# Optimization experiments

Hardware: AMD Instinct MI355X
Metric: run time of the kernel (lower is better)

Reference implementation:

```python
import jax, jax.numpy as jnp
import numpy as np
from jax import lax

WINDOW = 9
PAD = WINDOW // 2
LAMBDA_REG = 1.0
DN = lax.conv_dimension_numbers((1, 1, 1, 1, 1), (1, 1, 1, 1, 1), ('NCDHW', 'OIDHW', 'NCDHW'))


def _box_sum(x):
    """Sum over a 9x9x9 window with SAME padding, via separable 1D box filters.
    Mathematically identical to conv3d with an all-ones 9^3 kernel."""
    dtype = x.dtype
    for axis in range(3):  # D, H, W spatial axes
        kshape = [1, 1, 1, 1, 1]
        kshape[2 + axis] = WINDOW
        kernel = jnp.ones(kshape, dtype=dtype)
        padding = [(0, 0)] * 3
        padding[axis] = (PAD, PAD)
        x = lax.conv_general_dilated(x, kernel, window_strides=(1, 1, 1),
                                     padding=padding, dimension_numbers=DN)
    return x


def _lncc(I_fixed, I_moved):
    n = WINDOW ** 3
    fixed_sum = _box_sum(I_fixed)
    moved_sum = _box_sum(I_moved)
    fixed_mean = fixed_sum / n
    moved_mean = moved_sum / n
    fixed_sq = _box_sum(I_fixed * I_fixed)   # note: window SUM of squares (as in original)
    moved_sq = _box_sum(I_moved * I_moved)
    fixed_moved = _box_sum(I_fixed * I_moved)
    var_fixed = fixed_sq - fixed_mean ** 2
    var_moved = moved_sq - moved_mean ** 2
    cov = fixed_moved - fixed_mean * moved_mean
    cc = cov ** 2 / (var_fixed * var_moved + 1e-8)
    return -jnp.mean(cc)


def _gradient_loss(flow):
    dy = jnp.abs(flow[:, :, 1:, :, :] - flow[:, :, :-1, :, :])
    dx = jnp.abs(flow[:, :, :, 1:, :] - flow[:, :, :, :-1, :])
    dz = jnp.abs(flow[:, :, :, :, 1:] - flow[:, :, :, :, :-1])
    return jnp.mean(dx) + jnp.mean(dy) + jnp.mean(dz)


def setup_inputs() -> dict:
    key = jax.random.key(0)
    k1, k2, k3 = jax.random.split(key, 3)
    B, D, H, W = 2, 160, 192, 160
    I_fixed = jax.random.uniform(k1, (B, 1, D, H, W), dtype=jnp.float32)
    I_moved = jax.random.uniform(k2, (B, 1, D, H, W), dtype=jnp.float32)
    flow = jax.random.normal(k3, (B, 3, D, H, W), dtype=jnp.float32)
    return {"I_fixed": I_fixed, "I_moved": I_moved, "flow": flow}


def reference(I_fixed, I_moved, flow):
    L_sim = _lncc(I_fixed, I_moved)
    L_reg = _gradient_loss(flow)
    L_total = L_sim + LAMBDA_REG * L_reg
    return (L_total, L_sim, L_reg)
```

## Files before the change

### kernel.cpp

```cpp
#include <hip/hip_runtime.h>

#define Bz 2
#define Dz 160
#define Hz 192
#define Wz 160
#define HWl (Hz*Wz)
#define DHWl (Dz*Hz*Wz)

#define TH 16
#define TW 32
#define DT 32
#define RAWH (TH+8)
#define RAWW (TW+8)
#define NB_H (Hz/TH)
#define NB_W (Wz/TW)
#define NB_D (Dz/DT)
#define LNCC_BLOCKS (Bz*NB_H*NB_W*NB_D)
#define LNCC_THREADS 512
#define NSLICE (DT+8)

#define FLOW_BLOCKS 2048
#define FLOW_THREADS 256
#define FLOW_N4 ((Bz*3*DHWl)/4)

#define FPO LNCC_BLOCKS
#define WS_DOUBLES (FPO + 3*FLOW_BLOCKS)

__global__ __launch_bounds__(LNCC_THREADS, 2)
void lncc_kernel(const float* __restrict__ F, const float* __restrict__ M,
                 double* __restrict__ ws, int mode) {
    __shared__ float2 raw[RAWH][RAWW];
    __shared__ float4 wbv[RAWH][TW];
    __shared__ float  wbs[RAWH][TW];
    __shared__ double wred[LNCC_THREADS/64];

    const int bid = blockIdx.x;
    const int dc = bid % NB_D;
    const int wc = (bid / NB_D) % NB_W;
    const int hc = (bid / (NB_D * NB_W)) % NB_H;
    const int b  = bid / (NB_D * NB_W * NB_H);

    const int tid = threadIdx.x;
    const int th = tid >> 5;
    const int tw = tid & 31;

    const int h0 = hc * TH;
    const int w0 = wc * TW;
    const int d0 = dc * DT;
    const size_t bbase = (size_t)b * DHWl;

    float circ[9][5];
#pragma unroll
    for (int i = 0; i < 9; ++i)
#pragma unroll
        for (int j = 0; j < 5; ++j) circ[i][j] = 0.f;
    float rs0 = 0.f, rs1 = 0.f, rs2 = 0.f, rs3 = 0.f, rs4 = 0.f;
    float cc_acc = 0.f;

    for (int i0 = 0; i0 < NSLICE; i0 += 9) {
#pragma unroll
        for (int q = 0; q < 9; ++q) {
            const int i = i0 + q;
            if (i < NSLICE) {
                const int s = d0 - 4 + i;
                float nv0 = 0.f, nv1 = 0.f, nv2 = 0.f, nv3 = 0.f, nv4 = 0.f;
                if (s >= 0 && s < Dz) {
                    __syncthreads();
                    const size_t sbase = bbase + (size_t)s * HWl;
                    for (int k = tid; k < RAWH * RAWW; k += LNCC_THREADS) {
                        const int r = k / RAWW;
                        const int c = k - r * RAWW;
                        const int gh = h0 - 4 + r;
                        const int gw = w0 - 4 + c;
                        float fv = 0.f, mv = 0.f;
                        if (gh >= 0 && gh < Hz && gw >= 0 && gw < Wz) {
                            const size_t gi = sbase + (size_t)gh * Wz + gw;
                            fv = F[gi];
                            mv = M[gi];
                        }
                        raw[r][c] = make_float2(fv, mv);
                    }
                    __syncthreads();
                    for (int k = tid; k < RAWH * TW; k += LNCC_THREADS) {
                        const int r = k >> 5;
                        const int j = k & 31;
                        float sf = 0.f, sm = 0.f, sff = 0.f, smm = 0.f, sfm = 0.f;
#pragma unroll
                        for (int t = 0; t < 9; ++t) {
                            const float2 fm = raw[r][j + t];
                            sf  += fm.x;
                            sm  += fm.y;
                            sff += fm.x * fm.x;
                            smm += fm.y * fm.y;
                            sfm += fm.x * fm.y;
                        }
                        wbv[r][j] = make_float4(sf, sm, sff, smm);
                        wbs[r][j] = sfm;
                    }
                    __syncthreads();
#pragma unroll
                    for (int t = 0; t < 9; ++t) {
                        const float4 v = wbv[th + t][tw];
                        nv0 += v.x; nv1 += v.y; nv2 += v.z; nv3 += v.w;
                        nv4 += wbs[th + t][tw];
                    }
                }
                rs0 += nv0 - circ[q][0]; circ[q][0] = nv0;
                rs1 += nv1 - circ[q][1]; circ[q][1] = nv1;
                rs2 += nv2 - circ[q][2]; circ[q][2] = nv2;
                rs3 += nv3 - circ[q][3]; circ[q][3] = nv3;
                rs4 += nv4 - circ[q][4]; circ[q][4] = nv4;
                if (i >= 8) {
                    const float inv_n = 1.0f / 729.0f;
                    const float mf   = rs0 * inv_n;
                    const float mm   = rs1 * inv_n;
                    const float varf = rs2 - mf * mf;
                    const float varm = rs3 - mm * mm;
                    const float cov  = rs4 - mf * mm;
                    const float cc = cov * cov / (varf * varm + 1e-8f);
                    cc_acc += cc;
                }
            }
        }
    }

    double v = (double)cc_acc;
#pragma unroll
    for (int off = 32; off > 0; off >>= 1) v += __shfl_down(v, off);
    const int wave = tid >> 6, lane = tid & 63;
    if (lane == 0) wred[wave] = v;
    __syncthreads();
    if (tid == 0) {
        double t = 0.0;
        for (int k = 0; k < LNCC_THREADS / 64; ++k) t += wred[k];
        if (mode) ws[bid] = t;
        else      atomicAdd(&ws[0], t);
    }
}

__global__ __launch_bounds__(FLOW_THREADS)
void flow_grad_kernel(const float* __restrict__ X, double* __restrict__ ws, int mode) {
    __shared__ double wr0[4], wr1[4], wr2[4];
    float sd = 0.f, sh = 0.f, sw = 0.f;
    const int stride = gridDim.x * blockDim.x;
    for (int i4 = blockIdx.x * blockDim.x + threadIdx.x; i4 < FLOW_N4; i4 += stride) {
        const int base = i4 * 4;
        const float4 v = *(const float4*)(X + base);
        const int pos  = base % DHWl;
        const int w    = pos % Wz;
        const int rest = pos / Wz;
        const int h    = rest % Hz;
        const int d    = rest / Hz;
        float s = fabsf(v.y - v.x) + fabsf(v.z - v.y) + fabsf(v.w - v.z);
        if (w > 0) s += fabsf(v.x - X[base - 1]);
        sw += s;
        if (h > 0) {
            const float4 u = *(const float4*)(X + base - Wz);
            sh += fabsf(v.x - u.x) + fabsf(v.y - u.y) + fabsf(v.z - u.z) + fabsf(v.w - u.w);
        }
        if (d > 0) {
            const float4 u = *(const float4*)(X + base - HWl);
            sd += fabsf(v.x - u.x) + fabsf(v.y - u.y) + fabsf(v.z - u.z) + fabsf(v.w - u.w);
        }
    }
    double a = (double)sd, b = (double)sh, c = (double)sw;
#pragma unroll
    for (int off = 32; off > 0; off >>= 1) {
        a += __shfl_down(a, off);
        b += __shfl_down(b, off);
        c += __shfl_down(c, off);
    }
    const int wave = threadIdx.x >> 6, lane = threadIdx.x & 63;
    if (lane == 0) { wr0[wave] = a; wr1[wave] = b; wr2[wave] = c; }
    __syncthreads();
    if (threadIdx.x == 0) {
        double ta = 0.0, tb = 0.0, tc = 0.0;
        for (int k = 0; k < 4; ++k) { ta += wr0[k]; tb += wr1[k]; tc += wr2[k]; }
        if (mode) {
            double* p = ws + FPO + 3 * (size_t)blockIdx.x;
            p[0] = ta; p[1] = tb; p[2] = tc;
        } else {
            atomicAdd(&ws[1], ta);
            atomicAdd(&ws[2], tb);
            atomicAdd(&ws[3], tc);
        }
    }
}

__global__ __launch_bounds__(512)
void finalize_kernel(const double* __restrict__ ws, float* __restrict__ out, int mode) {
    __shared__ double red[4][8];
    double cc = 0.0, sd = 0.0, sh = 0.0, sw = 0.0;
    const int tid = threadIdx.x;
    if (mode) {
        for (int i = tid; i < LNCC_BLOCKS; i += 512) cc += ws[i];
        for (int i = tid; i < FLOW_BLOCKS; i += 512) {
            const double* p = ws + FPO + 3 * (size_t)i;
            sd += p[0]; sh += p[1]; sw += p[2];
        }
    } else if (tid == 0) {
        cc = ws[0]; sd = ws[1]; sh = ws[2]; sw = ws[3];
    }
#pragma unroll
    for (int off = 32; off > 0; off >>= 1) {
        cc += __shfl_down(cc, off);
        sd += __shfl_down(sd, off);
        sh += __shfl_down(sh, off);
        sw += __shfl_down(sw, off);
    }
    const int wave = tid >> 6, lane = tid & 63;
    if (lane == 0) { red[0][wave] = cc; red[1][wave] = sd; red[2][wave] = sh; red[3][wave] = sw; }
    __syncthreads();
    if (tid == 0) {
        double tcc = 0.0, tsd = 0.0, tsh = 0.0, tsw = 0.0;
        for (int k = 0; k < 8; ++k) {
            tcc += red[0][k]; tsd += red[1][k]; tsh += red[2][k]; tsw += red[3][k];
        }
        const double n_cc = 9830400.0;
        const double n_dx = 29337600.0;
        const double n_dy = 29306880.0;
        const double n_dz = 29306880.0;
        const double L_sim = -tcc / n_cc;
        const double L_reg = tsh / n_dx + tsd / n_dy + tsw / n_dz;
        out[0] = (float)(L_sim + L_reg);
        out[1] = (float)L_sim;
        out[2] = (float)L_reg;
    }
}

extern "C" void kernel_launch(void* const* d_in, const int* in_sizes, int n_in,
                              void* d_out, int out_size, void* d_ws, size_t ws_size,
                              hipStream_t stream) {
    (void)in_sizes; (void)n_in; (void)out_size;
    const float* F = (const float*)d_in[0];
    const float* M = (const float*)d_in[1];
    const float* X = (const float*)d_in[2];
    double* ws = (double*)d_ws;
    float* out = (float*)d_out;

    const int mode = (ws_size >= WS_DOUBLES * sizeof(double)) ? 1 : 0;
    if (!mode) hipMemsetAsync(d_ws, 0, 4 * sizeof(double), stream);

    lncc_kernel<<<LNCC_BLOCKS, LNCC_THREADS, 0, stream>>>(F, M, ws, mode);
    flow_grad_kernel<<<FLOW_BLOCKS, FLOW_THREADS, 0, stream>>>(X, ws, mode);
    finalize_kernel<<<1, 512, 0, stream>>>(ws, out, mode);
}
```

Baseline: 375.2 us.

## Shrink LNCC tiles, restructure flow gradient per slice, bucket atomics

Reduces the LNCC tile to 16x16 with a 20-deep D chunk and 256 threads, and pads the shared buffers. This raises the block count and parallelism but adds more halo reloads per output. The flow-gradient kernel now runs one block per (batch·channel, depth slice), removing the per-element div/mod. It takes the left neighbor via a lane shuffle instead of a scalar load. The fallback atomic path spreads accumulation over several buckets to cut atomic contention.

```diff
diff --git a/kernel.cpp b/kernel.cpp
--- a/kernel.cpp
+++ b/kernel.cpp
@@ -8,30 +8,32 @@
 #define DHWl (Dz*Hz*Wz)
 
 #define TH 16
-#define TW 32
-#define DT 32
+#define TW 16
+#define DT 20
 #define RAWH (TH+8)
 #define RAWW (TW+8)
 #define NB_H (Hz/TH)
 #define NB_W (Wz/TW)
 #define NB_D (Dz/DT)
 #define LNCC_BLOCKS (Bz*NB_H*NB_W*NB_D)
-#define LNCC_THREADS 512
+#define LNCC_THREADS 256
 #define NSLICE (DT+8)
 
-#define FLOW_BLOCKS 2048
+#define FLOW_BLOCKS (Bz*3*Dz)
 #define FLOW_THREADS 256
-#define FLOW_N4 ((Bz*3*DHWl)/4)
+#define W4 (Wz/4)
+#define SLICE_N4 (Hz*W4)
 
 #define FPO LNCC_BLOCKS
-#define WS_DOUBLES (FPO + 3*FLOW_BLOCKS)
+#define WS_MODE1_DBL (FPO + 3*FLOW_BLOCKS)
+#define MAXBUCK 64
 
 __global__ __launch_bounds__(LNCC_THREADS, 2)
 void lncc_kernel(const float* __restrict__ F, const float* __restrict__ M,
-                 double* __restrict__ ws, int mode) {
+                 double* __restrict__ ws, int nbuck, int mode) {
     __shared__ float2 raw[RAWH][RAWW];
-    __shared__ float4 wbv[RAWH][TW];
-    __shared__ float  wbs[RAWH][TW];
+    __shared__ float4 wbv[RAWH][TW + 1];
+    __shared__ float  wbs[RAWH][TW + 1];
     __shared__ double wred[LNCC_THREADS/64];
 
     const int bid = blockIdx.x;
@@ -41,8 +43,8 @@
     const int b  = bid / (NB_D * NB_W * NB_H);
 
     const int tid = threadIdx.x;
-    const int th = tid >> 5;
-    const int tw = tid & 31;
+    const int th = tid >> 4;
+    const int tw = tid & 15;
 
     const int h0 = hc * TH;
     const int w0 = wc * TW;
@@ -82,8 +84,8 @@
                     }
                     __syncthreads();
                     for (int k = tid; k < RAWH * TW; k += LNCC_THREADS) {
-                        const int r = k >> 5;
-                        const int j = k & 31;
+                        const int r = k >> 4;
+                        const int j = k & 15;
                         float sf = 0.f, sm = 0.f, sff = 0.f, smm = 0.f, sfm = 0.f;
 #pragma unroll
                         for (int t = 0; t < 9; ++t) {
@@ -134,32 +136,39 @@
         double t = 0.0;
         for (int k = 0; k < LNCC_THREADS / 64; ++k) t += wred[k];
         if (mode) ws[bid] = t;
-        else      atomicAdd(&ws[0], t);
+        else      atomicAdd(&ws[(bid % nbuck) * 4 + 0], t);
     }
 }
 
 __global__ __launch_bounds__(FLOW_THREADS)
-void flow_grad_kernel(const float* __restrict__ X, double* __restrict__ ws, int mode) {
+void flow_grad_kernel(const float* __restrict__ X, double* __restrict__ ws,
+                      int nbuck, int mode) {
     __shared__ double wr0[4], wr1[4], wr2[4];
+    const int fb = blockIdx.x;
+    const int d  = fb % Dz;
+    const int bc = fb / Dz;
+    const float* S = X + (size_t)bc * DHWl + (size_t)d * HWl;
+    const int lane = threadIdx.x & 63;
+
     float sd = 0.f, sh = 0.f, sw = 0.f;
-    const int stride = gridDim.x * blockDim.x;
-    for (int i4 = blockIdx.x * blockDim.x + threadIdx.x; i4 < FLOW_N4; i4 += stride) {
-        const int base = i4 * 4;
-        const float4 v = *(const float4*)(X + base);
-        const int pos  = base % DHWl;
-        const int w    = pos % Wz;
-        const int rest = pos / Wz;
-        const int h    = rest % Hz;
-        const int d    = rest / Hz;
+    for (int k4 = threadIdx.x; k4 < SLICE_N4; k4 += FLOW_THREADS) {
+        const int h  = k4 / W4;
+        const int w4 = k4 - h * W4;
+        const int base = h * Wz + w4 * 4;
+        const float4 v = *(const float4*)(S + base);
+        float left = __shfl_up(v.w, 1);
         float s = fabsf(v.y - v.x) + fabsf(v.z - v.y) + fabsf(v.w - v.z);
-        if (w > 0) s += fabsf(v.x - X[base - 1]);
+        if (w4 > 0) {
+            if (lane == 0) left = S[base - 1];
+            s += fabsf(v.x - left);
+        }
         sw += s;
         if (h > 0) {
-            const float4 u = *(const float4*)(X + base - Wz);
+            const float4 u = *(const float4*)(S + base - Wz);
             sh += fabsf(v.x - u.x) + fabsf(v.y - u.y) + fabsf(v.z - u.z) + fabsf(v.w - u.w);
         }
         if (d > 0) {
-            const float4 u = *(const float4*)(X + base - HWl);
+            const float4 u = *(const float4*)(S + base - HWl);
             sd += fabsf(v.x - u.x) + fabsf(v.y - u.y) + fabsf(v.z - u.z) + fabsf(v.w - u.w);
         }
     }
@@ -170,36 +179,39 @@
         b += __shfl_down(b, off);
         c += __shfl_down(c, off);
     }
-    const int wave = threadIdx.x >> 6, lane = threadIdx.x & 63;
+    const int wave = threadIdx.x >> 6;
     if (lane == 0) { wr0[wave] = a; wr1[wave] = b; wr2[wave] = c; }
     __syncthreads();
     if (threadIdx.x == 0) {
         double ta = 0.0, tb = 0.0, tc = 0.0;
         for (int k = 0; k < 4; ++k) { ta += wr0[k]; tb += wr1[k]; tc += wr2[k]; }
         if (mode) {
-            double* p = ws + FPO + 3 * (size_t)blockIdx.x;
+            double* p = ws + FPO + 3 * (size_t)fb;
             p[0] = ta; p[1] = tb; p[2] = tc;
         } else {
-            atomicAdd(&ws[1], ta);
-            atomicAdd(&ws[2], tb);
-            atomicAdd(&ws[3], tc);
+            double* p = ws + (fb % nbuck) * 4;
+            atomicAdd(&p[1], ta);
+            atomicAdd(&p[2], tb);
+            atomicAdd(&p[3], tc);
         }
     }
 }
 
 __global__ __launch_bounds__(512)
-void finalize_kernel(const double* __restrict__ ws, float* __restrict__ out, int mode) {
+void finalize_kernel(const double* __restrict__ ws, float* __restrict__ out,
+                     int nbuck, int mode) {
     __shared__ double red[4][8];
+    const int tid = threadIdx.x;
     double cc = 0.0, sd = 0.0, sh = 0.0, sw = 0.0;
-    const int tid = threadIdx.x;
     if (mode) {
         for (int i = tid; i < LNCC_BLOCKS; i += 512) cc += ws[i];
         for (int i = tid; i < FLOW_BLOCKS; i += 512) {
             const double* p = ws + FPO + 3 * (size_t)i;
             sd += p[0]; sh += p[1]; sw += p[2];
         }
-    } else if (tid == 0) {
-        cc = ws[0]; sd = ws[1]; sh = ws[2]; sw = ws[3];
+    } else if (tid < nbuck) {
+        const double* p = ws + tid * 4;
+        cc = p[0]; sd = p[1]; sh = p[2]; sw = p[3];
     }
 #pragma unroll
     for (int off = 32; off > 0; off >>= 1) {
@@ -238,10 +250,16 @@
     double* ws = (double*)d_ws;
     float* out = (float*)d_out;
 
-    const int mode = (ws_size >= WS_DOUBLES * sizeof(double)) ? 1 : 0;
-    if (!mode) hipMemsetAsync(d_ws, 0, 4 * sizeof(double), stream);
-
-    lncc_kernel<<<LNCC_BLOCKS, LNCC_THREADS, 0, stream>>>(F, M, ws, mode);
-    flow_grad_kernel<<<FLOW_BLOCKS, FLOW_THREADS, 0, stream>>>(X, ws, mode);
-    finalize_kernel<<<1, 512, 0, stream>>>(ws, out, mode);
-}
+    const int mode = (ws_size >= WS_MODE1_DBL * sizeof(double)) ? 1 : 0;
+    int nbuck = 1;
+    if (!mode) {
+        nbuck = (int)(ws_size / (4 * sizeof(double)));
+        if (nbuck > MAXBUCK) nbuck = MAXBUCK;
+        if (nbuck < 1) nbuck = 1;
+        hipMemsetAsync(d_ws, 0, (size_t)nbuck * 4 * sizeof(double), stream);
+    }
+
+    lncc_kernel<<<LNCC_BLOCKS, LNCC_THREADS, 0, stream>>>(F, M, ws, nbuck, mode);
+    flow_grad_kernel<<<FLOW_BLOCKS, FLOW_THREADS, 0, stream>>>(X, ws, nbuck, mode);
+    finalize_kernel<<<1, 512, 0, stream>>>(ws, out, nbuck, mode);
+}
```

After: 374.9 us. About the same (-0.1%).
